# Optimization experiments

Hardware: AMD Instinct MI355X
Metric: run time of the kernel (lower is better)

The kernel has to match this reference:

```python
import jax, jax.numpy as jnp
import numpy as np

B, S, D, H, OUT = 256, 256, 512, 512, 128  # batch, time points, state dim (= hidden_size), MLP hidden, out_features


def setup_inputs() -> dict:
    key = jax.random.key(0)
    ks = jax.random.split(key, 6)
    # time channel: shared monotone grid (forward uses t[0] as the integration grid)
    t = jnp.linspace(0.0, 1.0, S)
    feats = jax.random.normal(ks[0], (B, S, D), dtype=jnp.float32) * 0.1
    x = jnp.concatenate([jnp.broadcast_to(t[None, :, None], (B, S, 1)), feats], axis=-1)  # [B,S,D+1]
    s1 = 1.0 / np.sqrt(D).astype(np.float32)
    s2 = 1.0 / np.sqrt(H).astype(np.float32)
    W1 = jax.random.normal(ks[1], (H, D), dtype=jnp.float32) * s1
    b1 = jnp.zeros((H,), dtype=jnp.float32)
    W2 = jax.random.normal(ks[2], (D, H), dtype=jnp.float32) * s2
    b2 = jnp.zeros((D,), dtype=jnp.float32)
    Wout = jax.random.normal(ks[3], (OUT, H), dtype=jnp.float32) * s2
    bout = jnp.zeros((OUT,), dtype=jnp.float32)
    return dict(x=x, W1=W1, b1=b1, W2=W2, b2=b2, Wout=Wout, bout=bout)


def reference(x, W1, b1, W2, b2, Wout, bout):
    t = x[0, :, 0]          # [S] integration grid (first sample's time channel)
    y0 = x[:, -1, 1:]       # [B, D] initial state

    def f(y):               # ODEFunc MLP: d -> h -> d
        return jnp.tanh(y @ W1.T + b1) @ W2.T + b2

    dts = t[1:] - t[:-1]    # [S-1]

    def rk4_step(y, dt):
        k1 = f(y)
        k2 = f(y + 0.5 * dt * k1)
        k3 = f(y + 0.5 * dt * k2)
        k4 = f(y + dt * k3)
        y_next = y + (dt / 6.0) * (k1 + 2.0 * k2 + 2.0 * k3 + k4)
        return y_next, None

    yT, _ = jax.lax.scan(rk4_step, y0, dts)  # solution[-1]: [B, D]
    return yT @ Wout.T + bout                # [B, OUT]
```

## Files before the change

### kernel.cpp

```cpp
#include <hip/hip_runtime.h>
#include <hip/hip_bf16.h>

typedef __attribute__((ext_vector_type(8))) short short8;
typedef __attribute__((ext_vector_type(8))) unsigned short ushort8;
typedef __attribute__((ext_vector_type(4))) float f32x4;
typedef __attribute__((ext_vector_type(4))) int int4v;
typedef __attribute__((ext_vector_type(4))) short short4v;

#define NB 256
#define NS 256
#define NH 512
#define NOUT 128
#define XROW 513

#define NCL 16
#define RPC 16
#define BPC 4
#define UBS 128
#define LPAD 520

#define OFF_DTS   0
#define OFF_Y0    4096
#define OFF_U0    (OFF_Y0 + NB*NH*4)
#define OFF_M     (OFF_U0 + NB*NH*4)
#define OFF_C     (OFF_M + NH*NH*2)
#define OFF_P     (OFF_C + 4096)
#define OFF_HG    (OFF_P + NOUT*NH*4)
#define HG_BYTES  (NCL*2*RPC*NH*2)
#define OFF_HACC  (OFF_HG + HG_BYTES)
#define OFF_FLAGS (OFF_HACC + NB*NH*4)

static __device__ __forceinline__ unsigned bf16bits(float x) {
  return (unsigned)__builtin_bit_cast(unsigned short, __float2bfloat16(x));
}

static __device__ __forceinline__ void g_store8(void* addr, short4v v) {
  asm volatile("global_store_dwordx2 %0, %1, off sc0 sc1" :: "v"(addr), "v"(v) : "memory");
}
static __device__ __forceinline__ void g_store4(void* addr, unsigned v) {
  asm volatile("global_store_dword %0, %1, off sc0 sc1" :: "v"(addr), "v"(v) : "memory");
}
static __device__ __forceinline__ unsigned g_load4w(const void* addr) {
  unsigned v;
  asm volatile("global_load_dword %0, %1, off sc0 sc1\n\ts_waitcnt vmcnt(0)"
               : "=v"(v) : "v"(addr) : "memory");
  return v;
}
static __device__ __forceinline__ unsigned g_load4_nw(const void* addr) {
  unsigned v;
  asm volatile("global_load_dword %0, %1, off sc0 sc1" : "=v"(v) : "v"(addr) : "memory");
  return v;
}
static __device__ __forceinline__ void wait_vm0() {
  asm volatile("s_waitcnt vmcnt(0)" ::: "memory");
}
static __device__ __forceinline__ void bar_lgkm() {
  asm volatile("s_waitcnt lgkmcnt(0)" ::: "memory");
  __builtin_amdgcn_s_barrier();
}

static __device__ __forceinline__ float tanh_fast(float x) {
  x = fminf(fmaxf(x, -15.f), 15.f);
  float e = __expf(2.f * x);
  return (e - 1.f) * __builtin_amdgcn_rcpf(e + 1.f);
}


__global__ void k_dts(const float* __restrict__ x, float* __restrict__ dts) {
  int s = threadIdx.x;
  if (s < NS - 1) dts[s] = x[(s + 1) * XROW] - x[s * XROW];
  if (s == NS - 1) dts[NS - 1] = x[(NS - 1) * XROW] - x[0];
}

__global__ void k_y0(const float* __restrict__ x, float* __restrict__ y0) {
  int b = blockIdx.x;
  const float* src = x + (size_t)b * NS * XROW + (size_t)(NS - 1) * XROW + 1;
  for (int d = threadIdx.x; d < NH; d += blockDim.x) y0[b * NH + d] = src[d];
}

__global__ void k_c(const float* __restrict__ W1, const float* __restrict__ b2,
                    float* __restrict__ c) {
  int i = blockIdx.x * blockDim.x + threadIdx.x;
  if (i < NH) {
    float s = 0.f;
    for (int d = 0; d < NH; ++d) s += W1[i * NH + d] * b2[d];
    c[i] = s;
  }
}

__global__ void k_mm_nn_bf16(const float* __restrict__ A, const float* __restrict__ Bm,
                             __hip_bfloat16* __restrict__ C, int N, int K) {
  __shared__ float As[16][17], Bs[16][17];
  int tx = threadIdx.x & 15, ty = threadIdx.x >> 4;
  int m = blockIdx.y * 16 + ty, n = blockIdx.x * 16 + tx;
  float acc = 0.f;
  for (int k0 = 0; k0 < K; k0 += 16) {
    As[ty][tx] = A[m * K + k0 + tx];
    Bs[ty][tx] = Bm[(size_t)(k0 + ty) * N + n];
    __syncthreads();
#pragma unroll
    for (int kk = 0; kk < 16; ++kk) acc += As[ty][kk] * Bs[kk][tx];
    __syncthreads();
  }
  C[m * N + n] = __float2bfloat16(acc);
}

__global__ void k_mm_nn_f32(const float* __restrict__ A, const float* __restrict__ Bm,
                            float* __restrict__ C, int N, int K) {
  __shared__ float As[16][17], Bs[16][17];
  int tx = threadIdx.x & 15, ty = threadIdx.x >> 4;
  int m = blockIdx.y * 16 + ty, n = blockIdx.x * 16 + tx;
  float acc = 0.f;
  for (int k0 = 0; k0 < K; k0 += 16) {
    As[ty][tx] = A[m * K + k0 + tx];
    Bs[ty][tx] = Bm[(size_t)(k0 + ty) * N + n];
    __syncthreads();
#pragma unroll
    for (int kk = 0; kk < 16; ++kk) acc += As[ty][kk] * Bs[kk][tx];
    __syncthreads();
  }
  C[m * N + n] = acc;
}

__global__ void k_mm_nt_f32(const float* __restrict__ A, const float* __restrict__ Bm,
                            float* __restrict__ C, int N, int K) {
  __shared__ float As[16][17], Bs[16][17];
  int tx = threadIdx.x & 15, ty = threadIdx.x >> 4;
  int m = blockIdx.y * 16 + ty;
  int n0 = blockIdx.x * 16;
  float acc = 0.f;
  for (int k0 = 0; k0 < K; k0 += 16) {
    As[ty][tx] = A[m * K + k0 + tx];
    Bs[ty][tx] = Bm[(size_t)(n0 + ty) * K + k0 + tx];
    __syncthreads();
#pragma unroll
    for (int kk = 0; kk < 16; ++kk) acc += As[ty][kk] * Bs[tx][kk];
    __syncthreads();
  }
  C[m * N + n0 + tx] = acc;
}


__global__ __launch_bounds__(256) void k_main(
    const float* __restrict__ u0, const __hip_bfloat16* __restrict__ Mg,
    const float* __restrict__ cg, const float* __restrict__ b1g,
    const float* __restrict__ dtsg,
    __hip_bfloat16* __restrict__ hG, float* __restrict__ Hacc,
    unsigned int* __restrict__ flags)
{
  __shared__ __hip_bfloat16 hlds[RPC][LPAD];
  __shared__ float dtl[NS];

  const int tid = threadIdx.x;
  const int bx = blockIdx.x;
  const int xcd = bx & 7, slot = bx >> 3;
  const int cl = xcd + ((slot >> 2) << 3);
  const int jb = slot & 3;
  const int lane = tid & 63, wv = tid >> 6;
  const int r = lane & 15, g4 = lane >> 4;
  const int row0 = cl * RPC;
  const int ub = jb * UBS;
  const int rr = tid >> 4, sl = tid & 15;

  short8 Mreg[2][16];
#pragma unroll
  for (int t = 0; t < 2; ++t)
#pragma unroll
    for (int i = 0; i < 16; ++i) {
      int qg = ((jb + (i >> 2)) & 3) * 4 + (i & 3);
      Mreg[t][i] = *(const short8*)(Mg + (size_t)(ub + wv * 32 + t * 16 + r) * NH
                                    + qg * 32 + g4 * 8);
    }
  if (tid < NS) dtl[tid] = dtsg[tid];

  const int udl0 = wv * 32 + g4 * 4;
  float u[2][4], du[2][4], Ht[2][4], hr[2][4], wp[2][4], b1r[2][4], cr[2][4];
#pragma unroll
  for (int t = 0; t < 2; ++t)
#pragma unroll
    for (int j = 0; j < 4; ++j) {
      int ud = ub + udl0 + t * 16 + j;
      u[t][j] = u0[(row0 + r) * NH + ud];
      b1r[t][j] = b1g[ud];
      cr[t][j] = cg[ud];
      Ht[t][j] = 0.f; wp[t][j] = 0.f; du[t][j] = 0.f;
    }
  __syncthreads();

  unsigned int* flg = flags + cl * 32;
  const unsigned int* fp = flg + (lane & 15);
  const bool ownlane = (((lane & 15) >> 2) == jb);

  int sidx = 0;
  for (int step = 0; step < NS - 1; ++step) {
    float dt = dtl[step];
#pragma unroll 1
    for (int st = 0; st < 4; ++st, ++sidx) {
      float gam = (st == 0) ? 0.f : ((st == 3) ? dt : 0.5f * dt);
#pragma unroll
      for (int t = 0; t < 2; ++t)
#pragma unroll
        for (int j = 0; j < 4; ++j)
          hr[t][j] = tanh_fast(u[t][j] + gam * wp[t][j] + b1r[t][j]);

      int par = sidx & 1;
      __hip_bfloat16* hgp = hG + (size_t)(cl * 2 + par) * RPC * NH;
#pragma unroll
      for (int t = 0; t < 2; ++t) {
        short4v pk;
        pk.x = (short)bf16bits(hr[t][0]);
        pk.y = (short)bf16bits(hr[t][1]);
        pk.z = (short)bf16bits(hr[t][2]);
        pk.w = (short)bf16bits(hr[t][3]);
        int col = ub + udl0 + t * 16;
        g_store8(hgp + r * NH + col, pk);
        *(short4v*)&hlds[r][col] = pk;
      }
      bar_lgkm();

      unsigned tgt = (unsigned)(sidx + 1);
      unsigned specv = g_load4_nw(fp);

      f32x4 acc0 = {0.f, 0.f, 0.f, 0.f}, acc1 = {0.f, 0.f, 0.f, 0.f};
#pragma unroll
      for (int i = 0; i < 4; ++i) {
        int kc = ub + i * 32 + g4 * 8;
        short8 bf = *(const short8*)&hlds[r][kc];
        acc0 = __builtin_amdgcn_mfma_f32_16x16x32_bf16(Mreg[0][i], bf, acc0, 0, 0, 0);
        acc1 = __builtin_amdgcn_mfma_f32_16x16x32_bf16(Mreg[1][i], bf, acc1, 0, 0, 0);
      }

      wait_vm0();
      __builtin_amdgcn_sched_barrier(0);
      if (lane == 0) g_store4(flg + jb * 4 + wv, tgt);

      if (!__all((int)(ownlane || (specv >= tgt)))) {
        for (;;) {
          unsigned v = g_load4w(fp);
          if (__all((int)(ownlane || (v >= tgt)))) break;
          __builtin_amdgcn_s_sleep(1);
        }
      }

      {
        int4v d0, d1, d2;
        const __hip_bfloat16* hb = hgp + rr * NH;
        const void* a0 = hb + ((jb + 1) & 3) * UBS + sl * 8;
        const void* a1 = hb + ((jb + 2) & 3) * UBS + sl * 8;
        const void* a2 = hb + ((jb + 3) & 3) * UBS + sl * 8;
        asm volatile(
            "global_load_dwordx4 %0, %3, off sc0 sc1\n\t"
            "global_load_dwordx4 %1, %4, off sc0 sc1\n\t"
            "global_load_dwordx4 %2, %5, off sc0 sc1\n\t"
            "s_waitcnt vmcnt(0)"
            : "=&v"(d0), "=&v"(d1), "=&v"(d2)
            : "v"(a0), "v"(a1), "v"(a2)
            : "memory");
        *(int4v*)&hlds[rr][((jb + 1) & 3) * UBS + sl * 8] = d0;
        *(int4v*)&hlds[rr][((jb + 2) & 3) * UBS + sl * 8] = d1;
        *(int4v*)&hlds[rr][((jb + 3) & 3) * UBS + sl * 8] = d2;
      }
      __syncthreads();

#pragma unroll
      for (int m = 1; m < 4; ++m) {
        int jr = (jb + m) & 3;
#pragma unroll
        for (int qq = 0; qq < 4; ++qq) {
          int kc = jr * UBS + qq * 32 + g4 * 8;
          short8 bf = *(const short8*)&hlds[r][kc];
          acc0 = __builtin_amdgcn_mfma_f32_16x16x32_bf16(Mreg[0][m * 4 + qq], bf, acc0, 0, 0, 0);
          acc1 = __builtin_amdgcn_mfma_f32_16x16x32_bf16(Mreg[1][m * 4 + qq], bf, acc1, 0, 0, 0);
        }
      }

      {
        float cw = (st == 0 || st == 3) ? 1.f : 2.f;
        float f6 = dt * (1.f / 6.f);
        float f6c = f6 * cw;
#pragma unroll
        for (int j = 0; j < 4; ++j) {
          float w0 = acc0[j] + cr[0][j];
          float w1 = acc1[j] + cr[1][j];
          du[0][j] = (st == 0) ? w0 : du[0][j] + cw * w0;
          du[1][j] = (st == 0) ? w1 : du[1][j] + cw * w1;
          Ht[0][j] += f6c * hr[0][j];
          Ht[1][j] += f6c * hr[1][j];
          wp[0][j] = w0;
          wp[1][j] = w1;
        }
        if (st == 3) {
#pragma unroll
          for (int t = 0; t < 2; ++t)
#pragma unroll
            for (int j = 0; j < 4; ++j)
              u[t][j] += f6 * du[t][j];
        }
      }
    }
  }

#pragma unroll
  for (int t = 0; t < 2; ++t)
#pragma unroll
    for (int j = 0; j < 4; ++j)
      Hacc[(row0 + r) * NH + ub + udl0 + t * 16 + j] = Ht[t][j];
}

__global__ void k_epi(const float* __restrict__ y0, const float* __restrict__ Hacc,
                      const float* __restrict__ P, const float* __restrict__ Wout,
                      const float* __restrict__ b2, const float* __restrict__ bout,
                      const float* __restrict__ dtsg, float* __restrict__ out)
{
  __shared__ float ys[NH], hs[NH];
  int rr = blockIdx.x, o = threadIdx.x;
  float sdt = dtsg[NS - 1];
  for (int i = threadIdx.x; i < NH; i += blockDim.x) {
    ys[i] = y0[rr * NH + i] + sdt * b2[i];
    hs[i] = Hacc[rr * NH + i];
  }
  __syncthreads();
  float s = bout[o];
  const float* wr = Wout + o * NH;
  const float* pr = P + o * NH;
  for (int d = 0; d < NH; ++d) s += wr[d] * ys[d];
  for (int h = 0; h < NH; ++h) s += pr[h] * hs[h];
  out[rr * NOUT + o] = s;
}


extern "C" void kernel_launch(void* const* d_in, const int* in_sizes, int n_in,
                              void* d_out, int out_size, void* d_ws, size_t ws_size,
                              hipStream_t stream) {
  const float* x    = (const float*)d_in[0];
  const float* W1   = (const float*)d_in[1];
  const float* b1   = (const float*)d_in[2];
  const float* W2   = (const float*)d_in[3];
  const float* b2   = (const float*)d_in[4];
  const float* Wout = (const float*)d_in[5];
  const float* bout = (const float*)d_in[6];
  float* out = (float*)d_out;

  char* ws = (char*)d_ws;
  float*          dts  = (float*)(ws + OFF_DTS);
  float*          y0   = (float*)(ws + OFF_Y0);
  float*          u0   = (float*)(ws + OFF_U0);
  __hip_bfloat16* Mbf  = (__hip_bfloat16*)(ws + OFF_M);
  float*          cvec = (float*)(ws + OFF_C);
  float*          P    = (float*)(ws + OFF_P);
  __hip_bfloat16* hG   = (__hip_bfloat16*)(ws + OFF_HG);
  float*          Hac  = (float*)(ws + OFF_HACC);
  unsigned int*   flg  = (unsigned int*)(ws + OFF_FLAGS);

  hipMemsetAsync(flg, 0, NCL * 32 * 4, stream);

  k_dts<<<1, 256, 0, stream>>>(x, dts);
  k_y0 <<<NB, 256, 0, stream>>>(x, y0);
  k_c  <<<2, 256, 0, stream>>>(W1, b2, cvec);
  k_mm_nn_bf16<<<dim3(32, 32), 256, 0, stream>>>(W1, W2, Mbf, NH, NH);
  k_mm_nt_f32<<<dim3(32, 16), 256, 0, stream>>>(y0, W1, u0, NH, NH);
  k_mm_nn_f32<<<dim3(32, 8), 256, 0, stream>>>(Wout, W2, P, NH, NH);

  k_main<<<NCL * BPC, 256, 0, stream>>>(u0, Mbf, cvec, b1, dts, hG, Hac, flg);

  k_epi<<<NB, NOUT, 0, stream>>>(y0, Hac, P, Wout, b2, bout, dts, out);
}
```

Baseline: 2.463 ms.

## Split each row cluster across two blocks instead of four

Each 16-row cluster of the recurrent RK4 solve is now handled by 2 cooperating blocks, each owning half of the 512 hidden columns, instead of 4 blocks owning a quarter each. Each wave now keeps a 64x512 slice of M in registers. Per-stage cross-block exchange drops from three remote quarters to one remote half, and fewer blocks take part in each flag handshake. The cost is fewer active CUs (32 blocks), twice the MFMA work and register pressure per wave, and possible spills.

```diff
diff --git a/kernel.cpp b/kernel.cpp
--- a/kernel.cpp
+++ b/kernel.cpp
@@ -15,8 +15,7 @@
 
 #define NCL 16
 #define RPC 16
-#define BPC 4
-#define UBS 128
+#define NHALF 256
 #define LPAD 520
 
 #define OFF_DTS   0
@@ -141,7 +140,7 @@
 }
 
 
-__global__ __launch_bounds__(256) void k_main(
+__global__ __launch_bounds__(256, 1) void k_main(
     const float* __restrict__ u0, const __hip_bfloat16* __restrict__ Mg,
     const float* __restrict__ cg, const float* __restrict__ b1g,
     const float* __restrict__ dtsg,
@@ -153,33 +152,32 @@
 
   const int tid = threadIdx.x;
   const int bx = blockIdx.x;
-  const int xcd = bx & 7, slot = bx >> 3;
-  const int cl = xcd + ((slot >> 2) << 3);
-  const int jb = slot & 3;
+  const int cl = bx & 15, hb = bx >> 4;
   const int lane = tid & 63, wv = tid >> 6;
   const int r = lane & 15, g4 = lane >> 4;
   const int row0 = cl * RPC;
-  const int ub = jb * UBS;
+  const int rowbase = hb * NHALF + wv * 64;
+  const int ownbase = hb * NHALF;
+  const int peerbase = NHALF - ownbase;
   const int rr = tid >> 4, sl = tid & 15;
 
-  short8 Mreg[2][16];
-#pragma unroll
-  for (int t = 0; t < 2; ++t)
+  short8 Mreg[4][16];
+#pragma unroll
+  for (int t = 0; t < 4; ++t)
 #pragma unroll
     for (int i = 0; i < 16; ++i) {
-      int qg = ((jb + (i >> 2)) & 3) * 4 + (i & 3);
-      Mreg[t][i] = *(const short8*)(Mg + (size_t)(ub + wv * 32 + t * 16 + r) * NH
+      int qg = (i < 8) ? (hb * 8 + i) : ((1 - hb) * 8 + (i - 8));
+      Mreg[t][i] = *(const short8*)(Mg + (size_t)(rowbase + t * 16 + r) * NH
                                     + qg * 32 + g4 * 8);
     }
   if (tid < NS) dtl[tid] = dtsg[tid];
 
-  const int udl0 = wv * 32 + g4 * 4;
-  float u[2][4], du[2][4], Ht[2][4], hr[2][4], wp[2][4], b1r[2][4], cr[2][4];
-#pragma unroll
-  for (int t = 0; t < 2; ++t)
+  float u[4][4], du[4][4], Ht[4][4], hr[4][4], wp[4][4], b1r[4][4], cr[4][4];
+#pragma unroll
+  for (int t = 0; t < 4; ++t)
 #pragma unroll
     for (int j = 0; j < 4; ++j) {
-      int ud = ub + udl0 + t * 16 + j;
+      int ud = rowbase + t * 16 + g4 * 4 + j;
       u[t][j] = u0[(row0 + r) * NH + ud];
       b1r[t][j] = b1g[ud];
       cr[t][j] = cg[ud];
@@ -187,9 +185,9 @@
     }
   __syncthreads();
 
-  unsigned int* flg = flags + cl * 32;
-  const unsigned int* fp = flg + (lane & 15);
-  const bool ownlane = (((lane & 15) >> 2) == jb);
+  unsigned int* flg = flags + cl * 16;
+  const unsigned int* fp = flg + (lane & 7);
+  const bool ownlane = (((lane & 7) >> 2) == hb);
 
   int sidx = 0;
   for (int step = 0; step < NS - 1; ++step) {
@@ -198,7 +196,7 @@
     for (int st = 0; st < 4; ++st, ++sidx) {
       float gam = (st == 0) ? 0.f : ((st == 3) ? dt : 0.5f * dt);
 #pragma unroll
-      for (int t = 0; t < 2; ++t)
+      for (int t = 0; t < 4; ++t)
 #pragma unroll
         for (int j = 0; j < 4; ++j)
           hr[t][j] = tanh_fast(u[t][j] + gam * wp[t][j] + b1r[t][j]);
@@ -206,13 +204,13 @@
       int par = sidx & 1;
       __hip_bfloat16* hgp = hG + (size_t)(cl * 2 + par) * RPC * NH;
 #pragma unroll
-      for (int t = 0; t < 2; ++t) {
+      for (int t = 0; t < 4; ++t) {
         short4v pk;
         pk.x = (short)bf16bits(hr[t][0]);
         pk.y = (short)bf16bits(hr[t][1]);
         pk.z = (short)bf16bits(hr[t][2]);
         pk.w = (short)bf16bits(hr[t][3]);
-        int col = ub + udl0 + t * 16;
+        int col = rowbase + t * 16 + g4 * 4;
         g_store8(hgp + r * NH + col, pk);
         *(short4v*)&hlds[r][col] = pk;
       }
@@ -221,18 +219,21 @@
       unsigned tgt = (unsigned)(sidx + 1);
       unsigned specv = g_load4_nw(fp);
 
-      f32x4 acc0 = {0.f, 0.f, 0.f, 0.f}, acc1 = {0.f, 0.f, 0.f, 0.f};
-#pragma unroll
-      for (int i = 0; i < 4; ++i) {
-        int kc = ub + i * 32 + g4 * 8;
-        short8 bf = *(const short8*)&hlds[r][kc];
-        acc0 = __builtin_amdgcn_mfma_f32_16x16x32_bf16(Mreg[0][i], bf, acc0, 0, 0, 0);
-        acc1 = __builtin_amdgcn_mfma_f32_16x16x32_bf16(Mreg[1][i], bf, acc1, 0, 0, 0);
+      f32x4 acc[4];
+#pragma unroll
+      for (int t = 0; t < 4; ++t) acc[t] = (f32x4){0.f, 0.f, 0.f, 0.f};
+#pragma unroll
+      for (int i = 0; i < 8; ++i) {
+        short8 bf = *(const short8*)&hlds[r][ownbase + i * 32 + g4 * 8];
+        acc[0] = __builtin_amdgcn_mfma_f32_16x16x32_bf16(Mreg[0][i], bf, acc[0], 0, 0, 0);
+        acc[1] = __builtin_amdgcn_mfma_f32_16x16x32_bf16(Mreg[1][i], bf, acc[1], 0, 0, 0);
+        acc[2] = __builtin_amdgcn_mfma_f32_16x16x32_bf16(Mreg[2][i], bf, acc[2], 0, 0, 0);
+        acc[3] = __builtin_amdgcn_mfma_f32_16x16x32_bf16(Mreg[3][i], bf, acc[3], 0, 0, 0);
       }
 
       wait_vm0();
       __builtin_amdgcn_sched_barrier(0);
-      if (lane == 0) g_store4(flg + jb * 4 + wv, tgt);
+      if (lane == 0) g_store4(flg + hb * 4 + wv, tgt);
 
       if (!__all((int)(ownlane || (specv >= tgt)))) {
         for (;;) {
@@ -243,35 +244,29 @@
       }
 
       {
-        int4v d0, d1, d2;
-        const __hip_bfloat16* hb = hgp + rr * NH;
-        const void* a0 = hb + ((jb + 1) & 3) * UBS + sl * 8;
-        const void* a1 = hb + ((jb + 2) & 3) * UBS + sl * 8;
-        const void* a2 = hb + ((jb + 3) & 3) * UBS + sl * 8;
+        int4v d0, d1;
+        const __hip_bfloat16* hb0 = hgp + rr * NH + peerbase + sl * 16;
+        const void* a0 = hb0;
+        const void* a1 = hb0 + 8;
         asm volatile(
-            "global_load_dwordx4 %0, %3, off sc0 sc1\n\t"
-            "global_load_dwordx4 %1, %4, off sc0 sc1\n\t"
-            "global_load_dwordx4 %2, %5, off sc0 sc1\n\t"
+            "global_load_dwordx4 %0, %2, off sc0 sc1\n\t"
+            "global_load_dwordx4 %1, %3, off sc0 sc1\n\t"
             "s_waitcnt vmcnt(0)"
-            : "=&v"(d0), "=&v"(d1), "=&v"(d2)
-            : "v"(a0), "v"(a1), "v"(a2)
+            : "=&v"(d0), "=&v"(d1)
+            : "v"(a0), "v"(a1)
             : "memory");
-        *(int4v*)&hlds[rr][((jb + 1) & 3) * UBS + sl * 8] = d0;
-        *(int4v*)&hlds[rr][((jb + 2) & 3) * UBS + sl * 8] = d1;
-        *(int4v*)&hlds[rr][((jb + 3) & 3) * UBS + sl * 8] = d2;
+        *(int4v*)&hlds[rr][peerbase + sl * 16] = d0;
+        *(int4v*)&hlds[rr][peerbase + sl * 16 + 8] = d1;
       }
       __syncthreads();
 
 #pragma unroll
-      for (int m = 1; m < 4; ++m) {
-        int jr = (jb + m) & 3;
-#pragma unroll
-        for (int qq = 0; qq < 4; ++qq) {
-          int kc = jr * UBS + qq * 32 + g4 * 8;
-          short8 bf = *(const short8*)&hlds[r][kc];
-          acc0 = __builtin_amdgcn_mfma_f32_16x16x32_bf16(Mreg[0][m * 4 + qq], bf, acc0, 0, 0, 0);
-          acc1 = __builtin_amdgcn_mfma_f32_16x16x32_bf16(Mreg[1][m * 4 + qq], bf, acc1, 0, 0, 0);
-        }
+      for (int i = 8; i < 16; ++i) {
+        short8 bf = *(const short8*)&hlds[r][peerbase + (i - 8) * 32 + g4 * 8];
+        acc[0] = __builtin_amdgcn_mfma_f32_16x16x32_bf16(Mreg[0][i], bf, acc[0], 0, 0, 0);
+        acc[1] = __builtin_amdgcn_mfma_f32_16x16x32_bf16(Mreg[1][i], bf, acc[1], 0, 0, 0);
+        acc[2] = __builtin_amdgcn_mfma_f32_16x16x32_bf16(Mreg[2][i], bf, acc[2], 0, 0, 0);
+        acc[3] = __builtin_amdgcn_mfma_f32_16x16x32_bf16(Mreg[3][i], bf, acc[3], 0, 0, 0);
       }
 
       {
@@ -279,19 +274,17 @@
         float f6 = dt * (1.f / 6.f);
         float f6c = f6 * cw;
 #pragma unroll
-        for (int j = 0; j < 4; ++j) {
-          float w0 = acc0[j] + cr[0][j];
-          float w1 = acc1[j] + cr[1][j];
-          du[0][j] = (st == 0) ? w0 : du[0][j] + cw * w0;
-          du[1][j] = (st == 0) ? w1 : du[1][j] + cw * w1;
-          Ht[0][j] += f6c * hr[0][j];
-          Ht[1][j] += f6c * hr[1][j];
-          wp[0][j] = w0;
-          wp[1][j] = w1;
-        }
+        for (int t = 0; t < 4; ++t)
+#pragma unroll
+          for (int j = 0; j < 4; ++j) {
+            float wc = acc[t][j] + cr[t][j];
+            du[t][j] = (st == 0) ? wc : du[t][j] + cw * wc;
+            Ht[t][j] += f6c * hr[t][j];
+            wp[t][j] = wc;
+          }
         if (st == 3) {
 #pragma unroll
-          for (int t = 0; t < 2; ++t)
+          for (int t = 0; t < 4; ++t)
 #pragma unroll
             for (int j = 0; j < 4; ++j)
               u[t][j] += f6 * du[t][j];
@@ -301,10 +294,10 @@
   }
 
 #pragma unroll
-  for (int t = 0; t < 2; ++t)
+  for (int t = 0; t < 4; ++t)
 #pragma unroll
     for (int j = 0; j < 4; ++j)
-      Hacc[(row0 + r) * NH + ub + udl0 + t * 16 + j] = Ht[t][j];
+      Hacc[(row0 + r) * NH + rowbase + t * 16 + g4 * 4 + j] = Ht[t][j];
 }
 
 __global__ void k_epi(const float* __restrict__ y0, const float* __restrict__ Hacc,
@@ -352,7 +345,7 @@
   float*          Hac  = (float*)(ws + OFF_HACC);
   unsigned int*   flg  = (unsigned int*)(ws + OFF_FLAGS);
 
-  hipMemsetAsync(flg, 0, NCL * 32 * 4, stream);
+  hipMemsetAsync(flg, 0, NCL * 16 * 4, stream);
 
   k_dts<<<1, 256, 0, stream>>>(x, dts);
   k_y0 <<<NB, 256, 0, stream>>>(x, y0);
@@ -361,7 +354,7 @@
   k_mm_nt_f32<<<dim3(32, 16), 256, 0, stream>>>(y0, W1, u0, NH, NH);
   k_mm_nn_f32<<<dim3(32, 8), 256, 0, stream>>>(Wout, W2, P, NH, NH);
 
-  k_main<<<NCL * BPC, 256, 0, stream>>>(u0, Mbf, cvec, b1, dts, hG, Hac, flg);
+  k_main<<<NCL * 2, 256, 0, stream>>>(u0, Mbf, cvec, b1, dts, hG, Hac, flg);
 
   k_epi<<<NB, NOUT, 0, stream>>>(y0, Hac, P, Wout, b2, bout, dts, out);
 }
```

After: 3.052 ms. 23.9% more time.
